# Optimization experiments

Measured on AMD Instinct MI355X. Metric: run time of the kernel, lower is better.

The kernel has to match this reference:

```python
import jax, jax.numpy as jnp
import numpy as np

N_NODES = 20000
N_EDGES = 320000
D = 256          # out_channels (== in_channels here, so PyG zero-padding is a no-op)
NUM_LAYERS = 5


def setup_inputs() -> dict:
    key = jax.random.key(0)
    ks = jax.random.split(key, 8)
    x = jax.random.normal(ks[0], (N_NODES, D), dtype=jnp.float32)
    src = jax.random.randint(ks[1], (N_EDGES,), 0, N_NODES)
    dst = jax.random.randint(ks[2], (N_EDGES,), 0, N_NODES)
    edge_index = jnp.stack([src, dst]).astype(jnp.int64)
    edge_attr = jax.random.uniform(ks[3], (N_EDGES,), dtype=jnp.float32)
    s = 1.0 / np.sqrt(D)
    # per-layer message transform weights [L, D, D]
    weight = jax.random.uniform(ks[4], (NUM_LAYERS, D, D), minval=-s, maxval=s, dtype=jnp.float32)
    # GRUCell parameters (torch layout: [3*D, D] for W_ih/W_hh, [3*D] biases; gate order r, z, n)
    w_ih = jax.random.uniform(ks[5], (3 * D, D), minval=-s, maxval=s, dtype=jnp.float32)
    w_hh = jax.random.uniform(ks[6], (3 * D, D), minval=-s, maxval=s, dtype=jnp.float32)
    b = jax.random.uniform(ks[7], (2, 3 * D), minval=-s, maxval=s, dtype=jnp.float32)
    return {"x": x, "edge_index": edge_index, "edge_attr": edge_attr,
            "weight": weight, "w_ih": w_ih, "w_hh": w_hh,
            "b_ih": b[0], "b_hh": b[1]}


def gru_cell(m, h, w_ih, w_hh, b_ih, b_hh):
    gi = m @ w_ih.T + b_ih   # [N, 3D]
    gh = h @ w_hh.T + b_hh   # [N, 3D]
    i_r, i_z, i_n = jnp.split(gi, 3, axis=1)
    h_r, h_z, h_n = jnp.split(gh, 3, axis=1)
    r = jax.nn.sigmoid(i_r + h_r)
    z = jax.nn.sigmoid(i_z + h_z)
    n = jnp.tanh(i_n + r * h_n)
    return (1.0 - z) * n + z * h


def reference(x, edge_index, edge_attr, weight, w_ih, w_hh, b_ih, b_hh):
    src = edge_index[0]
    dst = edge_index[1]
    n_nodes = x.shape[0]
    h = x  # in_channels == out_channels, so no zero padding needed
    for i in range(weight.shape[0]):
        m = h @ weight[i]                                  # [N, D] transformed messages
        msgs = m[src] * edge_attr[:, None]                 # gather + edge weighting [E, D]
        agg = jax.ops.segment_sum(msgs, dst, num_segments=n_nodes)  # scatter-add [N, D]
        h = gru_cell(agg, h, w_ih, w_hh, b_ih, b_hh)
    return h
```

## Files before the change

### kernel.cpp

```cpp
#include <hip/hip_runtime.h>
#include <hip/hip_bf16.h>

#define NN 20000
#define NE 320000
#define DD 256

typedef __attribute__((ext_vector_type(8))) short bf16x8;
typedef __attribute__((ext_vector_type(4))) float f32x4;
typedef __attribute__((ext_vector_type(4))) int   int4v;
typedef __attribute__((ext_vector_type(4))) float float4v;

typedef __attribute__((address_space(1))) unsigned int gas_uint;
typedef __attribute__((address_space(3))) unsigned int las_uint;
static __device__ __forceinline__ void gload16(const void* g, void* l) {
    __builtin_amdgcn_global_load_lds((gas_uint*)g, (las_uint*)l, 16, 0, 0);
}

__device__ __forceinline__ unsigned short f2bf(float f) {
    union { float f; unsigned u; } v; v.f = f;
    unsigned r = v.u + 0x7fffu + ((v.u >> 16) & 1u);
    return (unsigned short)(r >> 16);
}
__device__ __forceinline__ float bf2f(unsigned short h) {
    union { unsigned u; float f; } v; v.u = ((unsigned)h) << 16;
    return v.f;
}
__device__ __forceinline__ float fast_sigmoid(float x) {
    return 1.f / (1.f + __expf(-x));
}
__device__ __forceinline__ float fast_tanh(float x) {
    x = fminf(fmaxf(x, -30.f), 30.f);
    float e = __expf(-2.f * x);
    return (1.f - e) / (1.f + e);
}


__global__ void cast_kernel(const float* __restrict__ in, unsigned short* __restrict__ out, int n) {
    int i = (blockIdx.x * blockDim.x + threadIdx.x) * 4;
    if (i >= n) return;
    float4v v = *reinterpret_cast<const float4v*>(in + i);
    uint2 o;
    o.x = (unsigned)f2bf(v.x) | ((unsigned)f2bf(v.y) << 16);
    o.y = (unsigned)f2bf(v.z) | ((unsigned)f2bf(v.w) << 16);
    *reinterpret_cast<uint2*>(out + i) = o;
}

__global__ __launch_bounds__(256) void pgemm_kernel(const unsigned short* __restrict__ A,
                                                    const unsigned short* __restrict__ Bt,
                                                    unsigned short* __restrict__ C) {
    __shared__ __align__(16) unsigned short As[128 * 64];
    __shared__ __align__(16) unsigned short Bs[64 * 64];
    const int t = threadIdx.x;
    const int lane = t & 63;
    const int w = t >> 6;
    const int wr = w >> 1, wc = w & 1;
    const int m0 = blockIdx.y * 128;
    const int n0 = blockIdx.x * 64;

    f32x4 acc[4][2];
    const f32x4 z4 = {0.f, 0.f, 0.f, 0.f};
    for (int i = 0; i < 4; ++i) for (int j = 0; j < 2; ++j) acc[i][j] = z4;

    for (int kt = 0; kt < 4; ++kt) {
        const int k0 = kt * 64;
#pragma unroll
        for (int rnd = 0; rnd < 4; ++rnd) {
            int cb = rnd * 256 + (w << 6);
            int c = cb + lane;
            int row = c >> 3, sl = c & 7;
            int gsl = sl ^ (row & 7);
            gload16(A + (size_t)(m0 + row) * 256 + k0 + gsl * 8, &As[cb * 8]);
        }
#pragma unroll
        for (int rnd = 0; rnd < 2; ++rnd) {
            int cb = rnd * 256 + (w << 6);
            int c = cb + lane;
            int row = c >> 3, sl = c & 7;
            int gsl = sl ^ (row & 7);
            gload16(Bt + (size_t)(n0 + row) * 256 + k0 + gsl * 8, &Bs[cb * 8]);
        }
        __syncthreads();
#pragma unroll
        for (int ks = 0; ks < 2; ++ks) {
            const int slot = ks * 4 + (lane >> 4);
            bf16x8 a[4], b[2];
#pragma unroll
            for (int mi = 0; mi < 4; ++mi) {
                int row = wr * 64 + mi * 16 + (lane & 15);
                a[mi] = *reinterpret_cast<const bf16x8*>(&As[row * 64 + ((slot ^ (row & 7)) << 3)]);
            }
#pragma unroll
            for (int ni = 0; ni < 2; ++ni) {
                int row = wc * 32 + ni * 16 + (lane & 15);
                b[ni] = *reinterpret_cast<const bf16x8*>(&Bs[row * 64 + ((slot ^ (row & 7)) << 3)]);
            }
#pragma unroll
            for (int mi = 0; mi < 4; ++mi)
#pragma unroll
                for (int ni = 0; ni < 2; ++ni)
                    acc[mi][ni] = __builtin_amdgcn_mfma_f32_16x16x32_bf16(a[mi], b[ni], acc[mi][ni], 0, 0, 0);
        }
        __syncthreads();
    }
#pragma unroll
    for (int mi = 0; mi < 4; ++mi)
#pragma unroll
        for (int ni = 0; ni < 2; ++ni)
#pragma unroll
            for (int r = 0; r < 4; ++r) {
                int grow = m0 + wr * 64 + mi * 16 + (lane >> 4) * 4 + r;
                int gcol = n0 + wc * 32 + ni * 16 + (lane & 15);
                C[(size_t)grow * 768 + gcol] = f2bf(acc[mi][ni][r]);
            }
}

__global__ void wc5_kernel(const unsigned short* __restrict__ Pall,
                           const float* __restrict__ whh,
                           unsigned short* __restrict__ Wc5) {
    int id = blockIdx.x * 256 + threadIdx.x;
    int k  = id & 255;
    int t2 = id >> 8;
    int n3 = t2 % 768;
    int t3 = t2 / 768;
    int hf = t3 & 1;
    int l  = t3 >> 1;
    int g3 = (n3 >> 4) % 3;
    int dg = n3 / 48;
    int dc = n3 & 15;
    int d  = dg * 16 + dc;
    int gate_row = g3 * 256 + d;
    unsigned short v;
    if (hf == 0) v = Pall[((size_t)(l * 256 + k)) * 768 + gate_row];
    else         v = f2bf(whh[(size_t)gate_row * 256 + k]);
    Wc5[id] = v;
}


__global__ void hist_kernel(const int* __restrict__ dst, int* __restrict__ deg) {
    int e = blockIdx.x * 256 + threadIdx.x;
    if (e < NE) atomicAdd(&deg[dst[e]], 1);
}

__global__ __launch_bounds__(1024) void scan_kernel(const int* __restrict__ deg, int* __restrict__ base) {
    __shared__ int part[1024];
    const int t = threadIdx.x;
    const int CH = 20;
    int start = t * CH;
    int s = 0;
    for (int i = 0; i < CH; ++i) { int idx = start + i; if (idx < NN) s += deg[idx]; }
    part[t] = s; __syncthreads();
    for (int off = 1; off < 1024; off <<= 1) {
        int v = (t >= off) ? part[t - off] : 0;
        __syncthreads();
        part[t] += v;
        __syncthreads();
    }
    int run = (t == 0) ? 0 : part[t - 1];
    for (int i = 0; i < CH; ++i) {
        int idx = start + i;
        if (idx < NN) { base[idx] = run; run += deg[idx]; }
    }
    if (t == 1023) base[NN] = run;
}

__global__ void fill_kernel(const int* __restrict__ src, const int* __restrict__ dst,
                            const float* __restrict__ attr, const int* __restrict__ base,
                            int* __restrict__ cursor, int* __restrict__ ssrc,
                            float* __restrict__ sattr) {
    int e = blockIdx.x * 256 + threadIdx.x;
    if (e >= NE) return;
    int d = dst[e];
    int pos = base[d] + atomicAdd(&cursor[d], 1);
    ssrc[pos] = src[e];
    sattr[pos] = attr[e];
}

__global__ __launch_bounds__(256) void gather_agg_kernel(const unsigned short* __restrict__ Hbf,
                                                         const int* __restrict__ base,
                                                         const int* __restrict__ ssrc,
                                                         const float* __restrict__ sattr,
                                                         unsigned short* __restrict__ AggBf) {
    int node = blockIdx.x * 4 + (threadIdx.x >> 6);
    if (node >= NN) return;
    int lane = threadIdx.x & 63;
    int q = lane >> 4;
    int ql = lane & 15;
    int b0 = base[node], b1 = base[node + 1];
    float ac[16];
#pragma unroll
    for (int j = 0; j < 16; ++j) ac[j] = 0.f;
    for (int p = b0 + q; p < b1; p += 4) {
        int s = ssrc[p];
        float a = sattr[p];
        const unsigned short* rowp = Hbf + (size_t)s * 256 + ql * 16;
        int4v v0 = *reinterpret_cast<const int4v*>(rowp);
        int4v v1 = *reinterpret_cast<const int4v*>(rowp + 8);
#pragma unroll
        for (int j = 0; j < 4; ++j) {
            unsigned u0 = (unsigned)v0[j];
            ac[2 * j]     += a * bf2f((unsigned short)(u0 & 0xffff));
            ac[2 * j + 1] += a * bf2f((unsigned short)(u0 >> 16));
            unsigned u1 = (unsigned)v1[j];
            ac[8 + 2 * j]     += a * bf2f((unsigned short)(u1 & 0xffff));
            ac[8 + 2 * j + 1] += a * bf2f((unsigned short)(u1 >> 16));
        }
    }
#pragma unroll
    for (int j = 0; j < 16; ++j) {
        ac[j] += __shfl_xor(ac[j], 16);
        ac[j] += __shfl_xor(ac[j], 32);
    }
    if (q == 0) {
        unsigned ou[8];
#pragma unroll
        for (int j = 0; j < 8; ++j)
            ou[j] = (unsigned)f2bf(ac[2 * j]) | ((unsigned)f2bf(ac[2 * j + 1]) << 16);
        unsigned short* op = AggBf + (size_t)node * 256 + ql * 16;
        *reinterpret_cast<int4v*>(op)     = *reinterpret_cast<int4v*>(&ou[0]);
        *reinterpret_cast<int4v*>(op + 8) = *reinterpret_cast<int4v*>(&ou[4]);
    }
}

__global__ __launch_bounds__(512) void gru4_kernel(const unsigned short* __restrict__ Abf,
                                                   const unsigned short* __restrict__ Hbf,
                                                   const unsigned short* __restrict__ Wc,
                                                   const float* __restrict__ b_ih,
                                                   const float* __restrict__ b_hh,
                                                   const float* __restrict__ x_f32,
                                                   float* __restrict__ h_out,
                                                   unsigned short* __restrict__ Hbf_out,
                                                   int first, int last) {
    __shared__ __align__(16) unsigned short As[128 * 64];
    __shared__ __align__(16) unsigned short Bs[96 * 64];
    const int t = threadIdx.x;
    const int lane = t & 63;
    const int w = t >> 6;
    const int wm = w >> 1, wn = w & 1;
    int b = blockIdx.x;
    int ww = (b & 7) * 158 + (b >> 3);
    const int mt = ww >> 3, dgp = ww & 7;
    const int m0 = mt * 128;

    f32x4 aR[2], aZ[2], aI[2], aH[2];
    const f32x4 z4 = {0.f, 0.f, 0.f, 0.f};
#pragma unroll
    for (int i = 0; i < 2; ++i) { aR[i] = z4; aZ[i] = z4; aI[i] = z4; aH[i] = z4; }

    auto do_half = [&](const unsigned short* __restrict__ aptr,
                       const unsigned short* __restrict__ wcb,
                       f32x4 (&aX)[2]) {
        for (int kq = 0; kq < 4; ++kq) {
            const int ka = kq * 64;
#pragma unroll
            for (int rnd = 0; rnd < 2; ++rnd) {
                int cb = rnd * 512 + (w << 6);
                int c = cb + lane;
                int row = c >> 3, sl = c & 7;
                int gsl = sl ^ (row & 7);
                gload16(aptr + (size_t)(m0 + row) * 256 + ka + gsl * 8, &As[cb * 8]);
            }
            {
                int cb = (w << 6);
                int c = cb + lane;
                int row = c >> 3, sl = c & 7;
                int gsl = sl ^ (row & 7);
                gload16(wcb + (size_t)(dgp * 96 + row) * 256 + ka + gsl * 8, &Bs[cb * 8]);
            }
            if (w < 4) {
                int cb = 512 + (w << 6);
                int c = cb + lane;
                int row = c >> 3, sl = c & 7;
                int gsl = sl ^ (row & 7);
                gload16(wcb + (size_t)(dgp * 96 + row) * 256 + ka + gsl * 8, &Bs[cb * 8]);
            }
            __syncthreads();
#pragma unroll
            for (int ks = 0; ks < 2; ++ks) {
                const int slot = ks * 4 + (lane >> 4);
                bf16x8 a[2], bfr[3];
#pragma unroll
                for (int mi = 0; mi < 2; ++mi) {
                    int row = wm * 32 + mi * 16 + (lane & 15);
                    a[mi] = *reinterpret_cast<const bf16x8*>(&As[row * 64 + ((slot ^ (row & 7)) << 3)]);
                }
#pragma unroll
                for (int g3 = 0; g3 < 3; ++g3) {
                    int row = wn * 48 + g3 * 16 + (lane & 15);
                    bfr[g3] = *reinterpret_cast<const bf16x8*>(&Bs[row * 64 + ((slot ^ (row & 7)) << 3)]);
                }
#pragma unroll
                for (int mi = 0; mi < 2; ++mi) {
                    aR[mi] = __builtin_amdgcn_mfma_f32_16x16x32_bf16(a[mi], bfr[0], aR[mi], 0, 0, 0);
                    aZ[mi] = __builtin_amdgcn_mfma_f32_16x16x32_bf16(a[mi], bfr[1], aZ[mi], 0, 0, 0);
                    aX[mi] = __builtin_amdgcn_mfma_f32_16x16x32_bf16(a[mi], bfr[2], aX[mi], 0, 0, 0);
                }
            }
            __syncthreads();
        }
    };

    do_half(Abf, Wc, aI);
    do_half(Hbf, Wc + 768 * 256, aH);

    const int d = (dgp * 2 + wn) * 16 + (lane & 15);
    const float bir = b_ih[d],        bhr = b_hh[d];
    const float biz = b_ih[256 + d],  bhz = b_hh[256 + d];
    const float bin_ = b_ih[512 + d], bhn = b_hh[512 + d];
#pragma unroll
    for (int mi = 0; mi < 2; ++mi)
#pragma unroll
        for (int r = 0; r < 4; ++r) {
            int grow = m0 + wm * 32 + mi * 16 + (lane >> 4) * 4 + r;
            if (grow >= NN) continue;
            size_t idx = (size_t)grow * 256 + d;
            float rr = fast_sigmoid(aR[mi][r] + bir + bhr);
            float zz = fast_sigmoid(aZ[mi][r] + biz + bhz);
            float nn = fast_tanh(aI[mi][r] + bin_ + rr * (aH[mi][r] + bhn));
            float hp = first ? x_f32[idx] : bf2f(Hbf[idx]);
            float hv = (1.f - zz) * nn + zz * hp;
            if (last) h_out[idx] = hv;
            Hbf_out[idx] = f2bf(hv);
        }
}


extern "C" void kernel_launch(void* const* d_in, const int* in_sizes, int n_in,
                              void* d_out, int out_size, void* d_ws, size_t ws_size,
                              hipStream_t stream) {
    const float* x     = (const float*)d_in[0];
    const int*   eidx  = (const int*)d_in[1];
    const float* eattr = (const float*)d_in[2];
    const float* W     = (const float*)d_in[3];
    const float* wih   = (const float*)d_in[4];
    const float* whh   = (const float*)d_in[5];
    const float* bih   = (const float*)d_in[6];
    const float* bhh   = (const float*)d_in[7];
    float* out = (float*)d_out;
    const int* esrc = eidx;
    const int* edst = eidx + NE;

    char* p = (char*)d_ws;
    auto alloc = [&](size_t bytes) -> char* {
        char* r = p; p += (bytes + 255) & ~(size_t)255; return r;
    };
    unsigned short* hbfA  = (unsigned short*)alloc((size_t)NN * DD * 2);
    unsigned short* hbfB  = (unsigned short*)alloc((size_t)NN * DD * 2);
    unsigned short* aggbf = (unsigned short*)alloc((size_t)NN * DD * 2);
    unsigned short* wnb   = (unsigned short*)alloc((size_t)5 * DD * DD * 2);
    unsigned short* wihb  = (unsigned short*)alloc((size_t)768 * DD * 2);
    unsigned short* pall  = (unsigned short*)alloc((size_t)1280 * 768 * 2);
    unsigned short* wc5   = (unsigned short*)alloc((size_t)5 * 2 * 768 * 256 * 2);
    int*   deg    = (int*)alloc((size_t)NN * 4);
    int*   basep  = (int*)alloc((size_t)(NN + 1) * 4);
    int*   cursor = (int*)alloc((size_t)NN * 4);
    int*   ssrc   = (int*)alloc((size_t)NE * 4);
    float* sattr  = (float*)alloc((size_t)NE * 4);
    alloc(262144);

    hipMemsetAsync(deg, 0, (size_t)NN * 4, stream);
    hipMemsetAsync(cursor, 0, (size_t)NN * 4, stream);

    cast_kernel<<<320, 256, 0, stream>>>(W, wnb, 5 * DD * DD);
    cast_kernel<<<192, 256, 0, stream>>>(wih, wihb, 768 * DD);
    cast_kernel<<<5000, 256, 0, stream>>>(x, hbfA, NN * DD);
    pgemm_kernel<<<dim3(12, 10), 256, 0, stream>>>(wnb, wihb, pall);
    wc5_kernel<<<7680, 256, 0, stream>>>(pall, whh, wc5);
    hist_kernel<<<1250, 256, 0, stream>>>(edst, deg);
    scan_kernel<<<1, 1024, 0, stream>>>(deg, basep);
    fill_kernel<<<1250, 256, 0, stream>>>(esrc, edst, eattr, basep, cursor, ssrc, sattr);

    unsigned short* hb_cur = hbfA;
    unsigned short* hb_nxt = hbfB;
    for (int l = 0; l < 5; ++l) {
        gather_agg_kernel<<<5000, 256, 0, stream>>>(hb_cur, basep, ssrc, sattr, aggbf);
        gru4_kernel<<<1264, 512, 0, stream>>>(aggbf, hb_cur, wc5 + (size_t)l * 2 * 768 * 256,
                                              bih, bhh, x, out, hb_nxt,
                                              (l == 0) ? 1 : 0, (l == 4) ? 1 : 0);
        unsigned short* tmp = hb_cur; hb_cur = hb_nxt; hb_nxt = tmp;
    }
    (void)in_sizes; (void)n_in; (void)out_size; (void)ws_size;
}
```

Before: 360.8 us.

## Fuse preprocessing casts, whh packing and degree histogram into one launch

```diff
diff --git a/kernel.cpp b/kernel.cpp
--- a/kernel.cpp
+++ b/kernel.cpp
@@ -34,20 +34,55 @@
     return (1.f - e) / (1.f + e);
 }
 
-
-__global__ void cast_kernel(const float* __restrict__ in, unsigned short* __restrict__ out, int n) {
-    int i = (blockIdx.x * blockDim.x + threadIdx.x) * 4;
-    if (i >= n) return;
-    float4v v = *reinterpret_cast<const float4v*>(in + i);
-    uint2 o;
-    o.x = (unsigned)f2bf(v.x) | ((unsigned)f2bf(v.y) << 16);
-    o.y = (unsigned)f2bf(v.z) | ((unsigned)f2bf(v.w) << 16);
-    *reinterpret_cast<uint2*>(out + i) = o;
+__global__ void prep_kernel(const float* __restrict__ x, unsigned short* __restrict__ hbfA,
+                            const float* __restrict__ W, unsigned short* __restrict__ wnb,
+                            const float* __restrict__ wih, unsigned short* __restrict__ wihb,
+                            const float* __restrict__ whh, unsigned short* __restrict__ wc5,
+                            const int* __restrict__ edst, int* __restrict__ deg) {
+    const int b = blockIdx.x, t = threadIdx.x;
+    if (b < 5000) {
+        int i = (b * 256 + t) * 4;
+        float4v v = *reinterpret_cast<const float4v*>(x + i);
+        uint2 o;
+        o.x = (unsigned)f2bf(v.x) | ((unsigned)f2bf(v.y) << 16);
+        o.y = (unsigned)f2bf(v.z) | ((unsigned)f2bf(v.w) << 16);
+        *reinterpret_cast<uint2*>(hbfA + i) = o;
+    } else if (b < 5320) {
+        int i = ((b - 5000) * 256 + t) * 4;
+        float4v v = *reinterpret_cast<const float4v*>(W + i);
+        uint2 o;
+        o.x = (unsigned)f2bf(v.x) | ((unsigned)f2bf(v.y) << 16);
+        o.y = (unsigned)f2bf(v.z) | ((unsigned)f2bf(v.w) << 16);
+        *reinterpret_cast<uint2*>(wnb + i) = o;
+    } else if (b < 5512) {
+        int i = ((b - 5320) * 256 + t) * 4;
+        float4v v = *reinterpret_cast<const float4v*>(wih + i);
+        uint2 o;
+        o.x = (unsigned)f2bf(v.x) | ((unsigned)f2bf(v.y) << 16);
+        o.y = (unsigned)f2bf(v.z) | ((unsigned)f2bf(v.w) << 16);
+        *reinterpret_cast<uint2*>(wihb + i) = o;
+    } else if (b < 5704) {
+        int id = (b - 5512) * 256 + t;
+        int n3 = id >> 6, k0 = (id & 63) * 4;
+        int g3 = (n3 >> 4) % 3;
+        int d = (n3 / 48) * 16 + (n3 & 15);
+        int gr = g3 * 256 + d;
+        float4v v = *reinterpret_cast<const float4v*>(whh + gr * 256 + k0);
+        uint2 o;
+        o.x = (unsigned)f2bf(v.x) | ((unsigned)f2bf(v.y) << 16);
+        o.y = (unsigned)f2bf(v.z) | ((unsigned)f2bf(v.w) << 16);
+#pragma unroll
+        for (int l = 0; l < 5; ++l)
+            *reinterpret_cast<uint2*>(wc5 + ((size_t)(l * 2 + 1) * 768 + n3) * 256 + k0) = o;
+    } else {
+        int e = (b - 5704) * 256 + t;
+        if (e < NE) atomicAdd(&deg[edst[e]], 1);
+    }
 }
 
 __global__ __launch_bounds__(256) void pgemm_kernel(const unsigned short* __restrict__ A,
                                                     const unsigned short* __restrict__ Bt,
-                                                    unsigned short* __restrict__ C) {
+                                                    unsigned short* __restrict__ wc5) {
     __shared__ __align__(16) unsigned short As[128 * 64];
     __shared__ __align__(16) unsigned short Bs[64 * 64];
     const int t = threadIdx.x;
@@ -110,36 +145,13 @@
             for (int r = 0; r < 4; ++r) {
                 int grow = m0 + wr * 64 + mi * 16 + (lane >> 4) * 4 + r;
                 int gcol = n0 + wc * 32 + ni * 16 + (lane & 15);
-                C[(size_t)grow * 768 + gcol] = f2bf(acc[mi][ni][r]);
-            }
-}
-
-__global__ void wc5_kernel(const unsigned short* __restrict__ Pall,
-                           const float* __restrict__ whh,
-                           unsigned short* __restrict__ Wc5) {
-    int id = blockIdx.x * 256 + threadIdx.x;
-    int k  = id & 255;
-    int t2 = id >> 8;
-    int n3 = t2 % 768;
-    int t3 = t2 / 768;
-    int hf = t3 & 1;
-    int l  = t3 >> 1;
-    int g3 = (n3 >> 4) % 3;
-    int dg = n3 / 48;
-    int dc = n3 & 15;
-    int d  = dg * 16 + dc;
-    int gate_row = g3 * 256 + d;
-    unsigned short v;
-    if (hf == 0) v = Pall[((size_t)(l * 256 + k)) * 768 + gate_row];
-    else         v = f2bf(whh[(size_t)gate_row * 256 + k]);
-    Wc5[id] = v;
-}
-
-
-__global__ void hist_kernel(const int* __restrict__ dst, int* __restrict__ deg) {
-    int e = blockIdx.x * 256 + threadIdx.x;
-    if (e < NE) atomicAdd(&deg[dst[e]], 1);
-}
+                int l = grow >> 8, k = grow & 255;
+                int g3 = gcol >> 8, d = gcol & 255;
+                int n3 = (d >> 4) * 48 + g3 * 16 + (d & 15);
+                wc5[((size_t)(l * 2) * 768 + n3) * 256 + k] = f2bf(acc[mi][ni][r]);
+            }
+}
+
 
 __global__ __launch_bounds__(1024) void scan_kernel(const int* __restrict__ deg, int* __restrict__ base) {
     __shared__ int part[1024];
@@ -348,24 +360,18 @@
     unsigned short* aggbf = (unsigned short*)alloc((size_t)NN * DD * 2);
     unsigned short* wnb   = (unsigned short*)alloc((size_t)5 * DD * DD * 2);
     unsigned short* wihb  = (unsigned short*)alloc((size_t)768 * DD * 2);
-    unsigned short* pall  = (unsigned short*)alloc((size_t)1280 * 768 * 2);
     unsigned short* wc5   = (unsigned short*)alloc((size_t)5 * 2 * 768 * 256 * 2);
-    int*   deg    = (int*)alloc((size_t)NN * 4);
+    int*   degcur = (int*)alloc((size_t)2 * NN * 4);
+    int*   deg    = degcur;
+    int*   cursor = degcur + NN;
     int*   basep  = (int*)alloc((size_t)(NN + 1) * 4);
-    int*   cursor = (int*)alloc((size_t)NN * 4);
     int*   ssrc   = (int*)alloc((size_t)NE * 4);
     float* sattr  = (float*)alloc((size_t)NE * 4);
     alloc(262144);
 
-    hipMemsetAsync(deg, 0, (size_t)NN * 4, stream);
-    hipMemsetAsync(cursor, 0, (size_t)NN * 4, stream);
-
-    cast_kernel<<<320, 256, 0, stream>>>(W, wnb, 5 * DD * DD);
-    cast_kernel<<<192, 256, 0, stream>>>(wih, wihb, 768 * DD);
-    cast_kernel<<<5000, 256, 0, stream>>>(x, hbfA, NN * DD);
-    pgemm_kernel<<<dim3(12, 10), 256, 0, stream>>>(wnb, wihb, pall);
-    wc5_kernel<<<7680, 256, 0, stream>>>(pall, whh, wc5);
-    hist_kernel<<<1250, 256, 0, stream>>>(edst, deg);
+    hipMemsetAsync(degcur, 0, (size_t)2 * NN * 4, stream);
+    prep_kernel<<<6954, 256, 0, stream>>>(x, hbfA, W, wnb, wih, wihb, whh, wc5, edst, deg);
+    pgemm_kernel<<<dim3(12, 10), 256, 0, stream>>>(wnb, wihb, wc5);
     scan_kernel<<<1, 1024, 0, stream>>>(deg, basep);
     fill_kernel<<<1250, 256, 0, stream>>>(esrc, edst, eattr, basep, cursor, ssrc, sattr);
 
```

Measured after the change: 343.8 us. 1.05x faster.
